# Kernel tuning notes

Measured on AMD Instinct MI355X. Metric: run time of the kernel, lower is better.

Reference implementation:

```python
import jax, jax.numpy as jnp
import numpy as np

T = 10            # inference steps (PCLayer.T)
LOCAL_LR = 0.001  # local_learning_rate
CLAMP = 1.0       # PCLayer.clamp_value


def setup_inputs() -> dict:
    key = jax.random.key(0)
    k1, k2 = jax.random.split(key)
    B, S, H_out, H_in = 8, 1024, 3072, 768
    target_activity = jax.random.normal(k1, (B, S, H_out), dtype=jnp.float32)
    # nn.Linear(H_in, H_out) weight: [H_out, H_in]
    W = jax.random.normal(k2, (H_out, H_in), dtype=jnp.float32) * (1.0 / np.sqrt(H_in))
    b = jnp.zeros((H_out,), dtype=jnp.float32)
    return {"target_activity": target_activity, "W": W, "b": b}


def reference(target_activity, W, b):
    # PCLayer forward, layer_type='fc1' (linear): T-step energy-gradient
    # fixed-point inference on latent x of shape [B, S, H_in].
    B, S, _ = target_activity.shape
    H_in = W.shape[1]
    x0 = jnp.zeros((B, S, H_in), dtype=target_activity.dtype)  # x_init

    def step(x, _):
        mu = jnp.einsum('bsi,oi->bso', x, W) + b       # prediction [B,S,H_out]
        err = target_activity - mu                      # prediction error
        # x <- x - lr * dE/dx, E = 0.5*||err||^2  =>  dE/dx = -err @ W
        x = x + LOCAL_LR * jnp.einsum('bso,oi->bsi', err, W)
        x = jnp.clip(x, -CLAMP, CLAMP)
        return x, None

    x, _ = jax.lax.scan(step, x0, None, length=T)
    return x
```

## Files before the change

kernel.cpp:

```cpp
#include <hip/hip_runtime.h>
#include <stdint.h>


typedef short bf16x8 __attribute__((ext_vector_type(8)));
typedef float f32x4  __attribute__((ext_vector_type(4)));
typedef unsigned short u16;
typedef unsigned int uint_as1 __attribute__((address_space(1)));
typedef unsigned int uint_as3 __attribute__((address_space(3)));

__device__ __forceinline__ float bf2f(u16 u) {
  union { unsigned int i; float f; } x; x.i = ((unsigned int)u) << 16; return x.f;
}
__device__ __forceinline__ u16 f2bf(float f) {
  union { float f; unsigned int i; } x; x.f = f;
  unsigned int r = x.i + 0x7fffu + ((x.i >> 16) & 1u);
  return (u16)(r >> 16);
}
__device__ __forceinline__ void gl2lds16(const void* g, void* l) {
  __builtin_amdgcn_global_load_lds((uint_as1*)(uintptr_t)g,
                                   (uint_as3*)(uintptr_t)l, 16, 0, 0);
}

template<int TM, int NK, int EPI>
__global__ __launch_bounds__(256, 2)
void gemm_lds(const u16* __restrict__ A, const u16* __restrict__ B,
              float* __restrict__ Cf, u16* __restrict__ Cb,
              const u16* __restrict__ Yb, float alpha, float beta,
              int K, int ldc, int kc, long zstride)
{
  constexpr int FM  = TM / 32;
  constexpr int RPW = TM / 4;
  __shared__ u16 As[TM * 32 * NK];
  __shared__ u16 Bs[128 * 32 * NK];
  const int tid = threadIdx.x, w = tid >> 6, lane = tid & 63;
  const int lm = lane & 15, quad = lane >> 4;
  const int wm = w & 1, wn = w >> 1;
  const int m0 = blockIdx.x * TM, n0 = blockIdx.y * 128;
  const long k0 = (long)blockIdx.z * kc;
  const int r = lane >> 2, q = lane & 3;
  const u16* Ag = A + (long)(m0 + w * RPW + r) * K + k0 + q * 8;
  const u16* Bg = B + (long)(n0 + w * 32 + r) * K + k0 + q * 8;
  u16* Asl = As + w * RPW * 32;
  u16* Bsl = Bs + w * 1024;

  f32x4 acc[FM][4] = {};

  for (int kk = 0; kk < kc; kk += 32 * NK) {
#pragma unroll
    for (int h = 0; h < NK; ++h) {
#pragma unroll
      for (int l = 0; l < RPW / 16; ++l)
        gl2lds16(Ag + (long)(l * 16) * K + kk + h * 32,
                 Asl + h * TM * 32 + l * 512);
      gl2lds16(Bg + kk + h * 32, Bsl + h * 4096);
      gl2lds16(Bg + 16 * (long)K + kk + h * 32, Bsl + h * 4096 + 512);
    }
    __syncthreads();
#pragma unroll
    for (int h = 0; h < NK; ++h) {
      bf16x8 af[FM], bv[4];
#pragma unroll
      for (int i = 0; i < FM; ++i)
        af[i] = *(const bf16x8*)(As + h * TM * 32 +
                                 (wm * (TM / 2) + i * 16 + lm) * 32 + quad * 8);
#pragma unroll
      for (int j = 0; j < 4; ++j)
        bv[j] = *(const bf16x8*)(Bs + h * 4096 +
                                 (wn * 64 + j * 16 + lm) * 32 + quad * 8);
#pragma unroll
      for (int i = 0; i < FM; ++i)
#pragma unroll
        for (int j = 0; j < 4; ++j)
          acc[i][j] = __builtin_amdgcn_mfma_f32_16x16x32_bf16(af[i], bv[j],
                                                              acc[i][j], 0, 0, 0);
    }
    __syncthreads();
  }

  const int rbase = m0 + wm * (TM / 2) + quad * 4;
  const int cbase = n0 + wn * 64 + lm;
  const long zoff = (long)blockIdx.z * zstride;
#pragma unroll
  for (int i = 0; i < FM; ++i)
#pragma unroll
    for (int j = 0; j < 4; ++j) {
      const int col = cbase + j * 16;
#pragma unroll
      for (int rr = 0; rr < 4; ++rr) {
        const long idx = (long)(rbase + i * 16 + rr) * ldc + col;
        const float v = alpha * acc[i][j][rr];
        if constexpr (EPI == 0)      Cf[zoff + idx] = v;
        else if constexpr (EPI == 1) Cb[idx] = f2bf(v);
        else                         Cf[idx] = v + beta * bf2f(Yb[idx]);
      }
    }
}

__global__ void conv_all(const float* __restrict__ t, const float* __restrict__ bias,
                         const float* __restrict__ W, u16* __restrict__ tb,
                         u16* __restrict__ WTb)
{
  __shared__ u16 lds[64 * 72];
  const int bx = blockIdx.x, tid = threadIdx.x;
  if (bx < 24576) {
    const long i4 = (long)bx * 256 + tid;
    const float4 v = ((const float4*)t)[i4];
    const float4 bb = ((const float4*)bias)[(int)(i4 % 768)];
    ushort4 o;
    o.x = f2bf(v.x - bb.x); o.y = f2bf(v.y - bb.y);
    o.z = f2bf(v.z - bb.z); o.w = f2bf(v.w - bb.w);
    ((ushort4*)tb)[i4] = o;
  } else {
    const int bt = bx - 24576;
    const int o0 = (bt / 12) * 64, i0 = (bt % 12) * 64;
    const int ol = tid >> 2, cg = tid & 3;
#pragma unroll
    for (int p = 0; p < 4; ++p) {
      const float4 v = *(const float4*)(W + (long)(o0 + ol) * 768 + i0 + (cg + p * 4) * 4);
      const int ib = (cg + p * 4) * 4;
      lds[(ib + 0) * 72 + ol] = f2bf(v.x);
      lds[(ib + 1) * 72 + ol] = f2bf(v.y);
      lds[(ib + 2) * 72 + ol] = f2bf(v.z);
      lds[(ib + 3) * 72 + ol] = f2bf(v.w);
    }
    __syncthreads();
    const int cl = tid >> 2, og = tid & 3;
    const u16* src = lds + cl * 72 + og * 16;
    u16* dst = WTb + (long)(i0 + cl) * 3072 + o0 + og * 16;
    ((ushort4*)dst)[0] = ((const ushort4*)src)[0];
    ((ushort4*)dst)[1] = ((const ushort4*)src)[1];
    ((ushort4*)dst)[2] = ((const ushort4*)src)[2];
    ((ushort4*)dst)[3] = ((const ushort4*)src)[3];
  }
}

__global__ void red_e(const float* __restrict__ R, float* __restrict__ Ef,
                      u16* __restrict__ Eb)
{
  const int i4 = blockIdx.x * 256 + threadIdx.x;
  float4 s = make_float4(0.f, 0.f, 0.f, 0.f);
#pragma unroll
  for (int z = 0; z < 6; ++z) {
    const float4 p = ((const float4*)R)[(long)z * 147456 + i4];
    s.x += p.x; s.y += p.y; s.z += p.z; s.w += p.w;
  }
  ((float4*)Ef)[i4] = s;
  ushort4 o; o.x = f2bf(s.x); o.y = f2bf(s.y); o.z = f2bf(s.z); o.w = f2bf(s.w);
  ((ushort4*)Eb)[i4] = o;
}

__global__ void red_s(const float* __restrict__ R, const float* __restrict__ Ef,
                      u16* __restrict__ Spb)
{
  const int i4 = blockIdx.x * 256 + threadIdx.x;
  float4 s = make_float4(0.f, 0.f, 0.f, 0.f);
#pragma unroll
  for (int z = 0; z < 6; ++z) {
    const float4 p = ((const float4*)R)[(long)z * 147456 + i4];
    s.x += p.x; s.y += p.y; s.z += p.z; s.w += p.w;
  }
  const float4 e = ((const float4*)Ef)[i4];
  ushort4 o;
  o.x = f2bf(-45.f * e.x + 120.f * s.x);
  o.y = f2bf(-45.f * e.y + 120.f * s.y);
  o.z = f2bf(-45.f * e.z + 120.f * s.z);
  o.w = f2bf(-45.f * e.w + 120.f * s.w);
  ((ushort4*)Spb)[i4] = o;
}

extern "C" void kernel_launch(void* const* d_in, const int* in_sizes, int n_in,
                              void* d_out, int out_size, void* d_ws, size_t ws_size,
                              hipStream_t stream)
{
  const float* t    = (const float*)d_in[0];
  const float* W    = (const float*)d_in[1];
  const float* bias = (const float*)d_in[2];
  float* out = (float*)d_out;

  char* p = (char*)d_ws;
  u16*   tb  = (u16*)(p + 0);
  u16*   WTb = (u16*)(p + 50331648);
  float* Ef  = (float*)(p + 55050240);
  u16*   Eb  = (u16*)(p + 57409536);
  u16*   Spb = (u16*)(p + 58589184);
  float* R   = (float*)(p + 59768832);
  u16*   yb  = (u16*)(p + 59768832);
  const float lr = 0.001f;

  conv_all<<<25152, 256, 0, stream>>>(t, bias, W, tb, WTb);
  gemm_lds<64, 2, 0><<<dim3(12, 6, 6), 256, 0, stream>>>(
      WTb, WTb, R, nullptr, nullptr, lr, 0.f, 3072, 768, 512, 589824);
  red_e<<<576, 256, 0, stream>>>(R, Ef, Eb);
  gemm_lds<64, 2, 0><<<dim3(12, 6, 6), 256, 0, stream>>>(
      Eb, Eb, R, nullptr, nullptr, 1.f, 0.f, 768, 768, 128, 589824);
  red_s<<<576, 256, 0, stream>>>(R, Ef, Spb);
  gemm_lds<128, 2, 1><<<dim3(64, 6, 1), 256, 0, stream>>>(
      tb, WTb, nullptr, yb, nullptr, 1.f, 0.f, 3072, 768, 3072, 0);
  gemm_lds<128, 2, 2><<<dim3(64, 6, 1), 256, 0, stream>>>(
      yb, Spb, out, nullptr, yb, lr, 0.01f, 768, 768, 768, 0);
}
```

Before: 271.3 us.

## Fold weight-only polynomial into combined matrix and fuse prep into cooperative kernel

Result: slower. 670.2 us (+147.0%).

```diff
diff --git a/kernel.cpp b/kernel.cpp
--- a/kernel.cpp
+++ b/kernel.cpp
@@ -1,5 +1,8 @@
 #include <hip/hip_runtime.h>
+#include <hip/hip_cooperative_groups.h>
 #include <stdint.h>
+
+namespace cgx = cooperative_groups;
 
 
 typedef short bf16x8 __attribute__((ext_vector_type(8)));
@@ -22,21 +25,21 @@
 }
 
 template<int TM, int NK, int EPI>
-__global__ __launch_bounds__(256, 2)
-void gemm_lds(const u16* __restrict__ A, const u16* __restrict__ B,
-              float* __restrict__ Cf, u16* __restrict__ Cb,
-              const u16* __restrict__ Yb, float alpha, float beta,
-              int K, int ldc, int kc, long zstride)
+__device__ __forceinline__
+void gemm_tile(u16* smem, const u16* __restrict__ A, const u16* __restrict__ B,
+               float* __restrict__ Cf, u16* __restrict__ Cb,
+               const u16* __restrict__ Yb, float alpha, float beta,
+               int K, int ldc, int kc, long zstride, int bx, int by, int bz)
 {
   constexpr int FM  = TM / 32;
   constexpr int RPW = TM / 4;
-  __shared__ u16 As[TM * 32 * NK];
-  __shared__ u16 Bs[128 * 32 * NK];
+  u16* As = smem;
+  u16* Bs = smem + TM * 32 * NK;
   const int tid = threadIdx.x, w = tid >> 6, lane = tid & 63;
   const int lm = lane & 15, quad = lane >> 4;
   const int wm = w & 1, wn = w >> 1;
-  const int m0 = blockIdx.x * TM, n0 = blockIdx.y * 128;
-  const long k0 = (long)blockIdx.z * kc;
+  const int m0 = bx * TM, n0 = by * 128;
+  const long k0 = (long)bz * kc;
   const int r = lane >> 2, q = lane & 3;
   const u16* Ag = A + (long)(m0 + w * RPW + r) * K + k0 + q * 8;
   const u16* Bg = B + (long)(n0 + w * 32 + r) * K + k0 + q * 8;
@@ -79,7 +82,7 @@
 
   const int rbase = m0 + wm * (TM / 2) + quad * 4;
   const int cbase = n0 + wn * 64 + lm;
-  const long zoff = (long)blockIdx.z * zstride;
+  const long zoff = (long)bz * zstride;
 #pragma unroll
   for (int i = 0; i < FM; ++i)
 #pragma unroll
@@ -89,83 +92,180 @@
       for (int rr = 0; rr < 4; ++rr) {
         const long idx = (long)(rbase + i * 16 + rr) * ldc + col;
         const float v = alpha * acc[i][j][rr];
-        if constexpr (EPI == 0)      Cf[zoff + idx] = v;
-        else if constexpr (EPI == 1) Cb[idx] = f2bf(v);
-        else                         Cf[idx] = v + beta * bf2f(Yb[idx]);
+        if constexpr (EPI == 0) Cf[zoff + idx] = v;
+        else                    Cb[idx] = f2bf(v + beta * bf2f(Yb[idx]));
       }
     }
 }
 
-__global__ void conv_all(const float* __restrict__ t, const float* __restrict__ bias,
-                         const float* __restrict__ W, u16* __restrict__ tb,
-                         u16* __restrict__ WTb)
-{
-  __shared__ u16 lds[64 * 72];
-  const int bx = blockIdx.x, tid = threadIdx.x;
-  if (bx < 24576) {
-    const long i4 = (long)bx * 256 + tid;
-    const float4 v = ((const float4*)t)[i4];
-    const float4 bb = ((const float4*)bias)[(int)(i4 % 768)];
-    ushort4 o;
-    o.x = f2bf(v.x - bb.x); o.y = f2bf(v.y - bb.y);
-    o.z = f2bf(v.z - bb.z); o.w = f2bf(v.w - bb.w);
-    ((ushort4*)tb)[i4] = o;
-  } else {
-    const int bt = bx - 24576;
+__global__ __launch_bounds__(256, 2)
+void prep_coop(const float* __restrict__ W, const float* __restrict__ bias,
+               u16* __restrict__ WTb, u16* __restrict__ Wb,
+               float* __restrict__ Ef, u16* __restrict__ Eb,
+               u16* __restrict__ Spb, float* __restrict__ R,
+               u16* __restrict__ WMTb, float* __restrict__ cvec)
+{
+  __shared__ u16 smem[12288];
+  cgx::grid_group grid = cgx::this_grid();
+  const int tid = threadIdx.x;
+  const float lr = 0.001f;
+
+  for (int bt = blockIdx.x; bt < 576; bt += gridDim.x) {
     const int o0 = (bt / 12) * 64, i0 = (bt % 12) * 64;
-    const int ol = tid >> 2, cg = tid & 3;
+    const int ol = tid >> 2, cg4 = tid & 3;
 #pragma unroll
     for (int p = 0; p < 4; ++p) {
-      const float4 v = *(const float4*)(W + (long)(o0 + ol) * 768 + i0 + (cg + p * 4) * 4);
-      const int ib = (cg + p * 4) * 4;
-      lds[(ib + 0) * 72 + ol] = f2bf(v.x);
-      lds[(ib + 1) * 72 + ol] = f2bf(v.y);
-      lds[(ib + 2) * 72 + ol] = f2bf(v.z);
-      lds[(ib + 3) * 72 + ol] = f2bf(v.w);
+      const float4 v = *(const float4*)(W + (long)(o0 + ol) * 768 + i0 + (cg4 + p * 4) * 4);
+      const int ib = (cg4 + p * 4) * 4;
+      smem[(ib + 0) * 72 + ol] = f2bf(v.x);
+      smem[(ib + 1) * 72 + ol] = f2bf(v.y);
+      smem[(ib + 2) * 72 + ol] = f2bf(v.z);
+      smem[(ib + 3) * 72 + ol] = f2bf(v.w);
+      ushort4 wo;
+      wo.x = f2bf(v.x); wo.y = f2bf(v.y); wo.z = f2bf(v.z); wo.w = f2bf(v.w);
+      ((ushort4*)(Wb + (long)(o0 + ol) * 768 + i0))[cg4 + p * 4] = wo;
     }
     __syncthreads();
     const int cl = tid >> 2, og = tid & 3;
-    const u16* src = lds + cl * 72 + og * 16;
+    const u16* src = smem + cl * 72 + og * 16;
     u16* dst = WTb + (long)(i0 + cl) * 3072 + o0 + og * 16;
     ((ushort4*)dst)[0] = ((const ushort4*)src)[0];
     ((ushort4*)dst)[1] = ((const ushort4*)src)[1];
     ((ushort4*)dst)[2] = ((const ushort4*)src)[2];
     ((ushort4*)dst)[3] = ((const ushort4*)src)[3];
-  }
-}
-
-__global__ void red_e(const float* __restrict__ R, float* __restrict__ Ef,
-                      u16* __restrict__ Eb)
-{
-  const int i4 = blockIdx.x * 256 + threadIdx.x;
-  float4 s = make_float4(0.f, 0.f, 0.f, 0.f);
-#pragma unroll
-  for (int z = 0; z < 6; ++z) {
-    const float4 p = ((const float4*)R)[(long)z * 147456 + i4];
-    s.x += p.x; s.y += p.y; s.z += p.z; s.w += p.w;
-  }
-  ((float4*)Ef)[i4] = s;
-  ushort4 o; o.x = f2bf(s.x); o.y = f2bf(s.y); o.z = f2bf(s.z); o.w = f2bf(s.w);
-  ((ushort4*)Eb)[i4] = o;
-}
-
-__global__ void red_s(const float* __restrict__ R, const float* __restrict__ Ef,
-                      u16* __restrict__ Spb)
-{
-  const int i4 = blockIdx.x * 256 + threadIdx.x;
-  float4 s = make_float4(0.f, 0.f, 0.f, 0.f);
-#pragma unroll
-  for (int z = 0; z < 6; ++z) {
-    const float4 p = ((const float4*)R)[(long)z * 147456 + i4];
-    s.x += p.x; s.y += p.y; s.z += p.z; s.w += p.w;
-  }
-  const float4 e = ((const float4*)Ef)[i4];
-  ushort4 o;
-  o.x = f2bf(-45.f * e.x + 120.f * s.x);
-  o.y = f2bf(-45.f * e.y + 120.f * s.y);
-  o.z = f2bf(-45.f * e.z + 120.f * s.z);
-  o.w = f2bf(-45.f * e.w + 120.f * s.w);
-  ((ushort4*)Spb)[i4] = o;
+    __syncthreads();
+  }
+  grid.sync();
+
+  if (blockIdx.x < 432) {
+    const int u = blockIdx.x;
+    gemm_tile<64, 2, 0>(smem, WTb, WTb, R, nullptr, nullptr, lr, 0.f,
+                        3072, 768, 512, 589824, u % 12, (u / 12) % 6, u / 72);
+  }
+  grid.sync();
+
+  for (int i4 = blockIdx.x * 256 + tid; i4 < 147456; i4 += gridDim.x * 256) {
+    float4 s = make_float4(0.f, 0.f, 0.f, 0.f);
+#pragma unroll
+    for (int z = 0; z < 6; ++z) {
+      const float4 p4 = ((const float4*)R)[(long)z * 147456 + i4];
+      s.x += p4.x; s.y += p4.y; s.z += p4.z; s.w += p4.w;
+    }
+    ((float4*)Ef)[i4] = s;
+    ushort4 o; o.x = f2bf(s.x); o.y = f2bf(s.y); o.z = f2bf(s.z); o.w = f2bf(s.w);
+    ((ushort4*)Eb)[i4] = o;
+  }
+  grid.sync();
+
+  if (blockIdx.x < 432) {
+    const int u = blockIdx.x;
+    gemm_tile<64, 2, 0>(smem, Eb, Eb, R, nullptr, nullptr, 1.f, 0.f,
+                        768, 768, 128, 589824, u % 12, (u / 12) % 6, u / 72);
+  }
+  grid.sync();
+
+  for (int i4 = blockIdx.x * 256 + tid; i4 < 147456; i4 += gridDim.x * 256) {
+    float4 s = make_float4(0.f, 0.f, 0.f, 0.f);
+#pragma unroll
+    for (int z = 0; z < 6; ++z) {
+      const float4 p4 = ((const float4*)R)[(long)z * 147456 + i4];
+      s.x += p4.x; s.y += p4.y; s.z += p4.z; s.w += p4.w;
+    }
+    const float4 e = ((const float4*)Ef)[i4];
+    ushort4 o;
+    o.x = f2bf(-45.f * e.x + 120.f * s.x);
+    o.y = f2bf(-45.f * e.y + 120.f * s.y);
+    o.z = f2bf(-45.f * e.z + 120.f * s.z);
+    o.w = f2bf(-45.f * e.w + 120.f * s.w);
+    ((ushort4*)Spb)[i4] = o;
+  }
+  grid.sync();
+
+  if (blockIdx.x < 288) {
+    const int u = blockIdx.x;
+    gemm_tile<64, 2, 3>(smem, Spb, Wb, nullptr, WMTb, WTb, lr, 0.01f,
+                        768, 3072, 768, 0, u % 12, u / 12, 0);
+  }
+  grid.sync();
+
+  if (blockIdx.x < 192) {
+    const int w = tid >> 6, lane = tid & 63;
+    const int row = blockIdx.x * 4 + w;
+    float s = 0.f;
+    for (int k = lane; k < 3072; k += 64)
+      s += bf2f(WMTb[(long)row * 3072 + k]) * bias[k];
+#pragma unroll
+    for (int off = 32; off; off >>= 1) s += __shfl_down(s, off);
+    if (lane == 0) cvec[row] = s;
+  }
+}
+
+__global__ __launch_bounds__(256, 2)
+void gemm_big(const float* __restrict__ T, const u16* __restrict__ B,
+              const float* __restrict__ cvec, float* __restrict__ out)
+{
+  __shared__ u16 As[2 * 64 * 32];
+  __shared__ u16 Bs[2 * 256 * 32];
+  const int tid = threadIdx.x, w = tid >> 6, lane = tid & 63;
+  const int lm = lane & 15, quad = lane >> 4;
+  const int m0 = blockIdx.x * 64, n0 = blockIdx.y * 256;
+  const int r = lane >> 2, q = lane & 3;
+  const u16* Bg = B + (long)(n0 + w * 64 + r) * 3072 + q * 8;
+  u16* Bsl = Bs + w * 64 * 32;
+  const int arow = tid >> 4, kq = tid & 15;
+  const float* Ag = T + (long)(m0 + arow) * 3072 + kq * 4;
+  const int h_a = kq >> 3, ks_a = (kq & 7) * 4;
+
+  f32x4 acc[4][4] = {};
+
+  for (int kk = 0; kk < 3072; kk += 64) {
+#pragma unroll
+    for (int h = 0; h < 2; ++h)
+#pragma unroll
+      for (int l = 0; l < 4; ++l)
+        gl2lds16(Bg + (long)(l * 16) * 3072 + kk + h * 32,
+                 Bsl + h * 8192 + l * 512);
+#pragma unroll
+    for (int p = 0; p < 4; ++p) {
+      const float4 v = *(const float4*)(Ag + (long)(p * 16) * 3072 + kk);
+      short4 o;
+      o.x = (short)f2bf(v.x); o.y = (short)f2bf(v.y);
+      o.z = (short)f2bf(v.z); o.w = (short)f2bf(v.w);
+      *(short4*)(As + h_a * 2048 + (arow + p * 16) * 32 + ks_a) = o;
+    }
+    __syncthreads();
+#pragma unroll
+    for (int h = 0; h < 2; ++h) {
+      bf16x8 af[4], bv[4];
+#pragma unroll
+      for (int i = 0; i < 4; ++i)
+        af[i] = *(const bf16x8*)(As + h * 2048 + (i * 16 + lm) * 32 + quad * 8);
+#pragma unroll
+      for (int j = 0; j < 4; ++j)
+        bv[j] = *(const bf16x8*)(Bs + h * 8192 + (w * 64 + j * 16 + lm) * 32 + quad * 8);
+#pragma unroll
+      for (int i = 0; i < 4; ++i)
+#pragma unroll
+        for (int j = 0; j < 4; ++j)
+          acc[i][j] = __builtin_amdgcn_mfma_f32_16x16x32_bf16(af[i], bv[j],
+                                                              acc[i][j], 0, 0, 0);
+    }
+    __syncthreads();
+  }
+
+  const int rbase = m0 + quad * 4;
+  const int cbase = n0 + w * 64 + lm;
+  float cj[4];
+#pragma unroll
+  for (int j = 0; j < 4; ++j) cj[j] = cvec[cbase + j * 16];
+#pragma unroll
+  for (int i = 0; i < 4; ++i)
+#pragma unroll
+    for (int j = 0; j < 4; ++j)
+#pragma unroll
+      for (int rr = 0; rr < 4; ++rr)
+        out[(long)(rbase + i * 16 + rr) * 768 + cbase + j * 16] =
+            acc[i][j][rr] - cj[j];
 }
 
 extern "C" void kernel_launch(void* const* d_in, const int* in_sizes, int n_in,
@@ -178,24 +278,18 @@
   float* out = (float*)d_out;
 
   char* p = (char*)d_ws;
-  u16*   tb  = (u16*)(p + 0);
-  u16*   WTb = (u16*)(p + 50331648);
-  float* Ef  = (float*)(p + 55050240);
-  u16*   Eb  = (u16*)(p + 57409536);
-  u16*   Spb = (u16*)(p + 58589184);
-  float* R   = (float*)(p + 59768832);
-  u16*   yb  = (u16*)(p + 59768832);
-  const float lr = 0.001f;
-
-  conv_all<<<25152, 256, 0, stream>>>(t, bias, W, tb, WTb);
-  gemm_lds<64, 2, 0><<<dim3(12, 6, 6), 256, 0, stream>>>(
-      WTb, WTb, R, nullptr, nullptr, lr, 0.f, 3072, 768, 512, 589824);
-  red_e<<<576, 256, 0, stream>>>(R, Ef, Eb);
-  gemm_lds<64, 2, 0><<<dim3(12, 6, 6), 256, 0, stream>>>(
-      Eb, Eb, R, nullptr, nullptr, 1.f, 0.f, 768, 768, 128, 589824);
-  red_s<<<576, 256, 0, stream>>>(R, Ef, Spb);
-  gemm_lds<128, 2, 1><<<dim3(64, 6, 1), 256, 0, stream>>>(
-      tb, WTb, nullptr, yb, nullptr, 1.f, 0.f, 3072, 768, 3072, 0);
-  gemm_lds<128, 2, 2><<<dim3(64, 6, 1), 256, 0, stream>>>(
-      yb, Spb, out, nullptr, yb, lr, 0.01f, 768, 768, 768, 0);
-}
+  u16*   WTb  = (u16*)(p + 0);
+  u16*   Wb   = (u16*)(p + 4718592);
+  float* Ef   = (float*)(p + 9437184);
+  u16*   Eb   = (u16*)(p + 11796480);
+  u16*   Spb  = (u16*)(p + 12976128);
+  float* R    = (float*)(p + 14155776);
+  u16*   WMTb = (u16*)(p + 28311552);
+  float* cvec = (float*)(p + 33030144);
+
+  void* args[] = {(void*)&W, (void*)&bias, (void*)&WTb, (void*)&Wb, (void*)&Ef,
+                  (void*)&Eb, (void*)&Spb, (void*)&R, (void*)&WMTb, (void*)&cvec};
+  hipLaunchCooperativeKernel((void*)prep_coop, dim3(512), dim3(256), args, 0, stream);
+
+  gemm_big<<<dim3(128, 3), 256, 0, stream>>>(t, WMTb, cvec, out);
+}
```
